# Kernel tuning notes

Hardware: AMD Instinct MI355X
Metric: run time of the kernel (lower is better)

## Reference

```python
import jax, jax.numpy as jnp
import numpy as np

N = 50000        # nodes
E_RAND = 800000  # random edges (self-loops appended -> E = 850000)
H = 8            # num_heads
D = 32           # h_feat_dim
IN = 128         # in_feat_dim
SM = 256         # sm_dim
SP = 128         # sp_dim
NEG_SLOPE = 0.2  # DGL GATv2Conv default


def setup_inputs() -> dict:
    key = jax.random.key(0)
    ks = jax.random.split(key, 16)
    s = 0.05
    self_loops = jnp.arange(N, dtype=jnp.int32)
    return {
        "sm_feats": jax.random.normal(ks[0], (N, SM), jnp.float32),
        "sp_feats": jax.random.normal(ks[1], (N, SP), jnp.float32),
        "src": jnp.concatenate([jax.random.randint(ks[2], (E_RAND,), 0, N, jnp.int32), self_loops]),
        "dst": jnp.concatenate([jax.random.randint(ks[3], (E_RAND,), 0, N, jnp.int32), self_loops]),
        # T1 / T2 linears
        "T1_w": jax.random.normal(ks[4], (SM, IN), jnp.float32) * s,
        "T1_b": jnp.zeros((IN,), jnp.float32),
        "T2_w": jax.random.normal(ks[5], (SP, IN), jnp.float32) * s,
        "T2_b": jnp.zeros((IN,), jnp.float32),
        # GATv2 layer 1: in = 2*IN
        "g1_src_w": jax.random.normal(ks[6], (2 * IN, H * D), jnp.float32) * s,
        "g1_dst_w": jax.random.normal(ks[7], (2 * IN, H * D), jnp.float32) * s,
        "g1_attn": jax.random.normal(ks[8], (H, D), jnp.float32) * s,
        "g1_bias": jnp.zeros((H * D,), jnp.float32),
        # GATv2 layer 2: in = D (after head-mean)
        "g2_src_w": jax.random.normal(ks[9], (D, H * D), jnp.float32) * s,
        "g2_dst_w": jax.random.normal(ks[10], (D, H * D), jnp.float32) * s,
        "g2_attn": jax.random.normal(ks[11], (H, D), jnp.float32) * s,
        "g2_bias": jnp.zeros((H * D,), jnp.float32),
    }


def gatv2_conv(x, src, dst, w_src, w_dst, attn, bias):
    # DGL GATv2Conv (share_weights=False, bias=True, no residual/activation)
    feat_src = (x @ w_src).reshape(-1, H, D)   # [N,H,D]
    feat_dst = (x @ w_dst).reshape(-1, H, D)   # [N,H,D]
    e = jax.nn.leaky_relu(feat_src[src] + feat_dst[dst], NEG_SLOPE)  # [E,H,D]
    score = jnp.einsum('ehd,hd->eh', e, attn)  # [E,H]
    # edge softmax over incoming edges per destination (self-loops ensure non-empty)
    smax = jax.ops.segment_max(score, dst, num_segments=N)           # [N,H]
    ex = jnp.exp(score - smax[dst])
    denom = jax.ops.segment_sum(ex, dst, num_segments=N)             # [N,H]
    alpha = ex / denom[dst]                                          # [E,H]
    out = jax.ops.segment_sum(alpha[:, :, None] * feat_src[src], dst, num_segments=N)  # [N,H,D]
    return out + bias.reshape(1, H, D)


def reference(sm_feats, sp_feats, src, dst,
              T1_w, T1_b, T2_w, T2_b,
              g1_src_w, g1_dst_w, g1_attn, g1_bias,
              g2_src_w, g2_dst_w, g2_attn, g2_bias):
    in_feat = jnp.concatenate([sm_feats @ T1_w + T1_b,
                               sp_feats @ T2_w + T2_b], axis=1)      # [N, 2*IN]
    h = gatv2_conv(in_feat, src, dst, g1_src_w, g1_dst_w, g1_attn, g1_bias)
    h = jax.nn.elu(h).mean(axis=1)                                   # [N, D]
    h = gatv2_conv(h, src, dst, g2_src_w, g2_dst_w, g2_attn, g2_bias)
    return h.mean(axis=1)                                            # [N, D]
```

## Files before the change

### kernel.cpp

```cpp
#include <hip/hip_runtime.h>
#include <hip/hip_fp16.h>


typedef unsigned int uint32;
typedef unsigned short u16;
typedef short short8 __attribute__((ext_vector_type(8)));
typedef float f32x4 __attribute__((ext_vector_type(4)));
typedef _Float16 f16x2 __attribute__((ext_vector_type(2)));

union H2 { f16x2 v; uint32 u; };

__device__ __forceinline__ uint32 bf_rne(uint32 u) { return (u + 0x7fffu + ((u >> 16) & 1u)) >> 16; }

__device__ __forceinline__ void split_trunc(float a, float b, uint32& h, uint32& l) {
  uint32 ua = __float_as_uint(a), ub = __float_as_uint(b);
  h = __builtin_amdgcn_perm(ub, ua, 0x07060302u);
  float ra = a - __uint_as_float(ua & 0xffff0000u);
  float rb = b - __uint_as_float(ub & 0xffff0000u);
  l = __builtin_amdgcn_perm(__float_as_uint(rb), __float_as_uint(ra), 0x07060302u);
}

__device__ __forceinline__ int wave_incl_scan(int x) {
  int lane = threadIdx.x & 63;
#pragma unroll
  for (int off = 1; off < 64; off <<= 1) {
    int t = __shfl_up(x, off, 64);
    if (lane >= off) x += t;
  }
  return x;
}

__global__ __launch_bounds__(256) void k_deg(const int* __restrict__ dst, int* __restrict__ deg, int E) {
  int e = blockIdx.x * 256 + threadIdx.x;
  if (e < E) atomicAdd(&deg[dst[e]], 1);
}

__global__ __launch_bounds__(256) void k_blkscan(const int* __restrict__ in, int* __restrict__ out,
                                                 int* __restrict__ blksum, int n) {
  __shared__ int wsum[4];
  int tid = threadIdx.x;
  int i0 = blockIdx.x * 1024 + tid * 4;
  int v0 = 0, v1 = 0, v2 = 0, v3 = 0;
  if (i0 + 3 < n) {
    int4 t = *(const int4*)(in + i0);
    v0 = t.x; v1 = t.y; v2 = t.z; v3 = t.w;
  } else {
    if (i0 < n) v0 = in[i0];
    if (i0 + 1 < n) v1 = in[i0 + 1];
    if (i0 + 2 < n) v2 = in[i0 + 2];
    if (i0 + 3 < n) v3 = in[i0 + 3];
  }
  int ts = v0 + v1 + v2 + v3;
  int incl = wave_incl_scan(ts);
  int lane = tid & 63, wid = tid >> 6;
  if (lane == 63) wsum[wid] = incl;
  __syncthreads();
  if (tid == 0) {
    int a = wsum[0], b = wsum[1], c = wsum[2], d = wsum[3];
    wsum[0] = 0; wsum[1] = a; wsum[2] = a + b; wsum[3] = a + b + c;
    blksum[blockIdx.x] = a + b + c + d;
  }
  __syncthreads();
  int excl = wsum[wid] + incl - ts;
  if (i0 + 3 < n) {
    int4 o; o.x = excl; o.y = excl + v0; o.z = excl + v0 + v1; o.w = excl + v0 + v1 + v2;
    *(int4*)(out + i0) = o;
  } else {
    if (i0 < n) out[i0] = excl;
    if (i0 + 1 < n) out[i0 + 1] = excl + v0;
    if (i0 + 2 < n) out[i0 + 2] = excl + v0 + v1;
    if (i0 + 3 < n) out[i0 + 3] = excl + v0 + v1 + v2;
  }
}

__global__ void k_scan_top(int* __restrict__ bs, int G) {
  int lane = threadIdx.x;
  int base = 0;
  for (int s = 0; s < G; s += 64) {
    int i = s + lane;
    int v = (i < G) ? bs[i] : 0;
    int incl = wave_incl_scan(v);
    if (i < G) bs[i] = base + incl - v;
    base += __shfl(incl, 63, 64);
  }
}

__global__ __launch_bounds__(256) void k_addoff(int* __restrict__ rp, const int* __restrict__ bs, int n, int Etot) {
  int i = blockIdx.x * 256 + threadIdx.x;
  if (i < n) rp[i] += bs[i >> 10];
  if (i == 0) rp[n] = Etot;
}

__global__ __launch_bounds__(256) void k_fill(const int* __restrict__ src, const int* __restrict__ dst,
                                              const int* __restrict__ rp, int* __restrict__ cnt,
                                              int* __restrict__ csr_src, int E) {
  int e = blockIdx.x * 256 + threadIdx.x;
  if (e < E) {
    int d = dst[e];
    int p = rp[d] + atomicAdd(&cnt[d], 1);
    csr_src[p] = src[e];
  }
}

__global__ __launch_bounds__(256) void k_precomb(const float* __restrict__ T1w, const float* __restrict__ T1b,
                                                 const float* __restrict__ T2w, const float* __restrict__ T2b,
                                                 const float* __restrict__ G, u16* __restrict__ Bh,
                                                 u16* __restrict__ Bl, float* __restrict__ cvec, int off) {
  int r = blockIdx.x;
  int j = threadIdx.x;
  float acc = 0.f;
  if (r < 256) {
    for (int m = 0; m < 128; m++) acc += T1w[r * 128 + m] * G[m * 256 + j];
  } else if (r < 384) {
    int rr = r - 256;
    for (int m = 0; m < 128; m++) acc += T2w[rr * 128 + m] * G[(128 + m) * 256 + j];
  } else {
    for (int m = 0; m < 128; m++) acc += T1b[m] * G[m * 256 + j] + T2b[m] * G[(128 + m) * 256 + j];
    cvec[off + j] = acc;
    return;
  }
  uint32 u = __float_as_uint(acc);
  uint32 hi = bf_rne(u);
  float rest = acc - __uint_as_float(hi << 16);
  uint32 lo = __float_as_uint(rest) >> 16;
  int k = r, colabs = off + j;
  int kt = k >> 5, lq = (k >> 3) & 3, j8 = k & 7;
  int cb = colabs >> 7, colr = colabs & 127, ni = colr >> 4, lr = colr & 15;
  size_t idx = ((size_t)(((cb * 12 + kt) * 8 + ni) * 4 + lq) * 16 + lr) * 8 + j8;
  Bh[idx] = (u16)hi;
  Bl[idx] = (u16)lo;
}

__global__ __launch_bounds__(256, 4) void k_gemm(const float* __restrict__ sm, const float* __restrict__ sp,
                                                 const u16* __restrict__ Bth, const u16* __restrict__ Btl,
                                                 const float* __restrict__ cvec, __half* __restrict__ fs,
                                                 __half* __restrict__ fd, int N) {
  __shared__ u16 BH[8192];
  __shared__ u16 BL[8192];
  int tid = threadIdx.x, w = tid >> 6, l = tid & 63;
  int lr = l & 15, lq = l >> 4;
  int cb = blockIdx.x, col0 = cb * 128, row0 = blockIdx.y * 128;
  int r0 = row0 + w * 32 + lr;
  int r1 = r0 + 16;
  int c0 = r0 < N ? r0 : N - 1;
  int c1 = r1 < N ? r1 : N - 1;

  f32x4 acc[2][8];
#pragma unroll
  for (int mt = 0; mt < 2; mt++)
#pragma unroll
    for (int ni = 0; ni < 8; ni++) acc[mt][ni] = (f32x4){0.f, 0.f, 0.f, 0.f};

  for (int st = 0; st < 6; st++) {
    int koff = st * 64;
    size_t g0 = (size_t)(cb * 12 + st * 2) * 4096;
    if (st) __syncthreads();
#pragma unroll
    for (int i = 0; i < 4; i++) {
      int c = i * 256 + tid;
      *(uint4*)&BH[c * 8] = *(const uint4*)(Bth + g0 + c * 8);
      *(uint4*)&BL[c * 8] = *(const uint4*)(Btl + g0 + c * 8);
    }
    __syncthreads();
#pragma unroll
    for (int t = 0; t < 2; t++) {
      int kk = koff + t * 32;
      int ks = kk + lq * 8;
      const float* ga0 = (kk < 256) ? (sm + (size_t)c0 * 256 + ks) : (sp + (size_t)c0 * 128 + (ks - 256));
      const float* ga1 = (kk < 256) ? (sm + (size_t)c1 * 256 + ks) : (sp + (size_t)c1 * 128 + (ks - 256));
      float4 v00 = *(const float4*)(ga0);
      float4 v01 = *(const float4*)(ga0 + 4);
      float4 v10 = *(const float4*)(ga1);
      float4 v11 = *(const float4*)(ga1 + 4);
      uint4 H0, L0, H1, L1;
      split_trunc(v00.x, v00.y, H0.x, L0.x);
      split_trunc(v00.z, v00.w, H0.y, L0.y);
      split_trunc(v01.x, v01.y, H0.z, L0.z);
      split_trunc(v01.z, v01.w, H0.w, L0.w);
      split_trunc(v10.x, v10.y, H1.x, L1.x);
      split_trunc(v10.z, v10.w, H1.y, L1.y);
      split_trunc(v11.x, v11.y, H1.z, L1.z);
      split_trunc(v11.z, v11.w, H1.w, L1.w);
      short8 a0h = *(short8*)&H0, a0l = *(short8*)&L0;
      short8 a1h = *(short8*)&H1, a1l = *(short8*)&L1;
#pragma unroll
      for (int ni = 0; ni < 8; ni++) {
        int lo = ((t * 8 + ni) * 64 + l) * 8;
        short8 bh = *(const short8*)&BH[lo];
        short8 bl = *(const short8*)&BL[lo];
        acc[0][ni] = __builtin_amdgcn_mfma_f32_16x16x32_bf16(a0h, bh, acc[0][ni], 0, 0, 0);
        acc[0][ni] = __builtin_amdgcn_mfma_f32_16x16x32_bf16(a0l, bh, acc[0][ni], 0, 0, 0);
        acc[0][ni] = __builtin_amdgcn_mfma_f32_16x16x32_bf16(a0h, bl, acc[0][ni], 0, 0, 0);
        acc[1][ni] = __builtin_amdgcn_mfma_f32_16x16x32_bf16(a1h, bh, acc[1][ni], 0, 0, 0);
        acc[1][ni] = __builtin_amdgcn_mfma_f32_16x16x32_bf16(a1l, bh, acc[1][ni], 0, 0, 0);
        acc[1][ni] = __builtin_amdgcn_mfma_f32_16x16x32_bf16(a1h, bl, acc[1][ni], 0, 0, 0);
      }
    }
  }
#pragma unroll
  for (int mt = 0; mt < 2; mt++) {
    int rb = row0 + w * 32 + mt * 16 + lq * 4;
#pragma unroll
    for (int ni = 0; ni < 8; ni++) {
      int c = col0 + ni * 16 + lr;
      float cv = cvec[c];
      __half* op = fs; int cc = c;
      if (c >= 256) { op = fd; cc = c - 256; }
#pragma unroll
      for (int r = 0; r < 4; r++) {
        int rr = rb + r;
        if (rr < N) op[(size_t)rr * 256 + cc] = __float2half(acc[mt][ni][r] + cv);
      }
    }
  }
}

__global__ __launch_bounds__(256) void k_feat2(const float* __restrict__ h, const float* __restrict__ Ws,
                                               const float* __restrict__ Wd, __half* __restrict__ fs,
                                               __half* __restrict__ fd, int N) {
  int j = threadIdx.x;
  int n0 = blockIdx.x * 32;
  float ws[32], wd[32];
#pragma unroll
  for (int k = 0; k < 32; k++) {
    ws[k] = Ws[k * 256 + j];
    wd[k] = Wd[k * 256 + j];
  }
  int nend = n0 + 32; if (nend > N) nend = N;
#pragma unroll 2
  for (int n = n0; n < nend; n++) {
    const float* hr = h + (size_t)n * 32;
    float as = 0.f, ad = 0.f;
#pragma unroll
    for (int k = 0; k < 32; k++) {
      float hv = hr[k];
      as += hv * ws[k];
      ad += hv * wd[k];
    }
    fs[(size_t)n * 256 + j] = __float2half(as);
    fd[(size_t)n * 256 + j] = __float2half(ad);
  }
}

template <int FINAL>
__global__ __launch_bounds__(256) void k_edge(const uint2* __restrict__ fs, const uint2* __restrict__ fd,
                                              const int* __restrict__ csr_src, const int* __restrict__ rp,
                                              const float* __restrict__ attn, const float* __restrict__ bias,
                                              float* __restrict__ out, int N) {
  int n = blockIdx.x * 4 + (threadIdx.x >> 6);
  if (n >= N) return;
  int lane = threadIdx.x & 63;
  float4 av = ((const float4*)attn)[lane];
  H2 AV01, AV23, Y01, Y23;
  AV01.v = (f16x2){(_Float16)av.x, (_Float16)av.y};
  AV23.v = (f16x2){(_Float16)av.z, (_Float16)av.w};
  const f16x2 c02 = {(_Float16)0.2f, (_Float16)0.2f};
  uint2 yu = fd[(size_t)n * 64 + lane];
  Y01.u = yu.x; Y23.u = yu.y;
  int beg = rp[n], end = rp[n + 1];
  float den0 = 0.f, den1 = 0.f;
  float4 acc0 = {0.f, 0.f, 0.f, 0.f}, acc1 = {0.f, 0.f, 0.f, 0.f};
  int e = beg;
  for (; e + 2 <= end; e += 2) {
    int s0 = csr_src[e], s1 = csr_src[e + 1];
    uint2 xu0 = fs[(size_t)s0 * 64 + lane];
    uint2 xu1 = fs[(size_t)s1 * 64 + lane];
    H2 Xa, Xb, Xc, Xd;
    Xa.u = xu0.x; Xb.u = xu0.y; Xc.u = xu1.x; Xd.u = xu1.y;
    f16x2 ea0 = Xa.v + Y01.v, eb0 = Xb.v + Y23.v;
    f16x2 ea1 = Xc.v + Y01.v, eb1 = Xd.v + Y23.v;
    f16x2 ta0 = __builtin_elementwise_max(ea0, ea0 * c02);
    f16x2 tb0 = __builtin_elementwise_max(eb0, eb0 * c02);
    f16x2 ta1 = __builtin_elementwise_max(ea1, ea1 * c02);
    f16x2 tb1 = __builtin_elementwise_max(eb1, eb1 * c02);
    float p0 = __builtin_amdgcn_fdot2(ta0, AV01.v, 0.f, false);
    float p1 = __builtin_amdgcn_fdot2(ta1, AV01.v, 0.f, false);
    p0 = __builtin_amdgcn_fdot2(tb0, AV23.v, p0, false);
    p1 = __builtin_amdgcn_fdot2(tb1, AV23.v, p1, false);
    p0 += __shfl_xor(p0, 1, 64); p1 += __shfl_xor(p1, 1, 64);
    p0 += __shfl_xor(p0, 2, 64); p1 += __shfl_xor(p1, 2, 64);
    p0 += __shfl_xor(p0, 4, 64); p1 += __shfl_xor(p1, 4, 64);
    float w0 = __expf(p0), w1 = __expf(p1);
    den0 += w0; den1 += w1;
    acc0.x += w0 * (float)Xa.v.x; acc0.y += w0 * (float)Xa.v.y;
    acc0.z += w0 * (float)Xb.v.x; acc0.w += w0 * (float)Xb.v.y;
    acc1.x += w1 * (float)Xc.v.x; acc1.y += w1 * (float)Xc.v.y;
    acc1.z += w1 * (float)Xd.v.x; acc1.w += w1 * (float)Xd.v.y;
  }
  if (e < end) {
    int s0 = csr_src[e];
    uint2 xu0 = fs[(size_t)s0 * 64 + lane];
    H2 Xa, Xb; Xa.u = xu0.x; Xb.u = xu0.y;
    f16x2 ea0 = Xa.v + Y01.v, eb0 = Xb.v + Y23.v;
    f16x2 ta0 = __builtin_elementwise_max(ea0, ea0 * c02);
    f16x2 tb0 = __builtin_elementwise_max(eb0, eb0 * c02);
    float p0 = __builtin_amdgcn_fdot2(ta0, AV01.v, 0.f, false);
    p0 = __builtin_amdgcn_fdot2(tb0, AV23.v, p0, false);
    p0 += __shfl_xor(p0, 1, 64);
    p0 += __shfl_xor(p0, 2, 64);
    p0 += __shfl_xor(p0, 4, 64);
    float w0 = __expf(p0);
    den0 += w0;
    acc0.x += w0 * (float)Xa.v.x; acc0.y += w0 * (float)Xa.v.y;
    acc0.z += w0 * (float)Xb.v.x; acc0.w += w0 * (float)Xb.v.y;
  }
  float4 acc = {acc0.x + acc1.x, acc0.y + acc1.y, acc0.z + acc1.z, acc0.w + acc1.w};
  float invd = 1.f / (den0 + den1);
  float4 b = ((const float4*)bias)[lane];
  acc.x = acc.x * invd + b.x;
  acc.y = acc.y * invd + b.y;
  acc.z = acc.z * invd + b.z;
  acc.w = acc.w * invd + b.w;
  if (!FINAL) {
    acc.x = acc.x > 0.f ? acc.x : expm1f(acc.x);
    acc.y = acc.y > 0.f ? acc.y : expm1f(acc.y);
    acc.z = acc.z > 0.f ? acc.z : expm1f(acc.z);
    acc.w = acc.w > 0.f ? acc.w : expm1f(acc.w);
  }
#pragma unroll
  for (int mask = 8; mask <= 32; mask <<= 1) {
    acc.x += __shfl_xor(acc.x, mask, 64);
    acc.y += __shfl_xor(acc.y, mask, 64);
    acc.z += __shfl_xor(acc.z, mask, 64);
    acc.w += __shfl_xor(acc.w, mask, 64);
  }
  if (lane < 8) {
    float4 o = {acc.x * 0.125f, acc.y * 0.125f, acc.z * 0.125f, acc.w * 0.125f};
    ((float4*)out)[(size_t)n * 8 + lane] = o;
  }
}

extern "C" void kernel_launch(void* const* d_in, const int* in_sizes, int n_in,
                              void* d_out, int out_size, void* d_ws, size_t ws_size,
                              hipStream_t stream) {
  const float* sm  = (const float*)d_in[0];
  const float* sp  = (const float*)d_in[1];
  const int*   src = (const int*)d_in[2];
  const int*   dst = (const int*)d_in[3];
  const float* T1w = (const float*)d_in[4];
  const float* T1b = (const float*)d_in[5];
  const float* T2w = (const float*)d_in[6];
  const float* T2b = (const float*)d_in[7];
  const float* g1sw = (const float*)d_in[8];
  const float* g1dw = (const float*)d_in[9];
  const float* g1a  = (const float*)d_in[10];
  const float* g1b  = (const float*)d_in[11];
  const float* g2sw = (const float*)d_in[12];
  const float* g2dw = (const float*)d_in[13];
  const float* g2a  = (const float*)d_in[14];
  const float* g2b  = (const float*)d_in[15];
  const int N = in_sizes[1] / 128;
  const int E = in_sizes[2];
  float* out = (float*)d_out;

  size_t off = 0;
  char* wsb = (char*)d_ws;
  auto alloc = [&](size_t bytes) -> void* {
    void* p = wsb + off;
    off += (bytes + 255) & ~(size_t)255;
    return p;
  };
  u16* Bth = (u16*)alloc((size_t)512 * 384 * 2);
  u16* Btl = (u16*)alloc((size_t)512 * 384 * 2);
  float* cvec  = (float*)alloc(512 * 4);
  int* deg     = (int*)alloc((size_t)N * 4);
  int* cnt     = (int*)alloc((size_t)N * 4);
  int* row_ptr = (int*)alloc((size_t)(N + 1) * 4);
  int* blksum  = (int*)alloc(4096 * 4);
  int* csr_src = (int*)alloc((size_t)E * 4);
  __half* fs   = (__half*)alloc((size_t)N * 256 * 2);
  __half* fd   = (__half*)alloc((size_t)N * 256 * 2);
  float* hmid  = (float*)alloc((size_t)N * 32 * 4);
  (void)ws_size; (void)n_in; (void)out_size;

  (void)hipMemsetAsync(deg, 0, (size_t)N * 4, stream);
  (void)hipMemsetAsync(cnt, 0, (size_t)N * 4, stream);

  k_deg<<<(E + 255) / 256, 256, 0, stream>>>(dst, deg, E);
  int nblk = (N + 1023) / 1024;
  k_blkscan<<<nblk, 256, 0, stream>>>(deg, row_ptr, blksum, N);
  k_scan_top<<<1, 64, 0, stream>>>(blksum, nblk);
  k_addoff<<<(N + 255) / 256, 256, 0, stream>>>(row_ptr, blksum, N, E);
  k_fill<<<(E + 255) / 256, 256, 0, stream>>>(src, dst, row_ptr, cnt, csr_src, E);

  k_precomb<<<385, 256, 0, stream>>>(T1w, T1b, T2w, T2b, g1sw, Bth, Btl, cvec, 0);
  k_precomb<<<385, 256, 0, stream>>>(T1w, T1b, T2w, T2b, g1dw, Bth, Btl, cvec, 256);

  dim3 ggrid(4, (N + 127) / 128);
  k_gemm<<<ggrid, 256, 0, stream>>>(sm, sp, Bth, Btl, cvec, fs, fd, N);
  k_edge<0><<<(N + 3) / 4, 256, 0, stream>>>((const uint2*)fs, (const uint2*)fd, csr_src, row_ptr, g1a, g1b, hmid, N);

  k_feat2<<<(N + 31) / 32, 256, 0, stream>>>(hmid, g2sw, g2dw, fs, fd, N);
  k_edge<1><<<(N + 3) / 4, 256, 0, stream>>>((const uint2*)fs, (const uint2*)fd, csr_src, row_ptr, g2a, g2b, out, N);
}
```

Baseline: 508.7 us.

## Double-buffer GEMM with async LDS loads, swizzle blocks, prefetch edge gathers

The GEMM now double-buffers the B tiles in shared memory and fills them with global_load_lds, while register-prefetching the next A stage so loads overlap the MFMA work. Its launch becomes a 1D grid with a swizzled block-to-tile mapping that groups the four column blocks of nearby row blocks, and occupancy is lowered to 2 blocks per CU. The edge kernel gathers four source rows ahead of the compute for the previous four, hiding gather latency at the cost of more registers. The two precombine launches are merged into one.

New measurement: 498.5 us. -2.0%, faster.

```diff
diff --git a/kernel.cpp b/kernel.cpp
--- a/kernel.cpp
+++ b/kernel.cpp
@@ -104,9 +104,13 @@
 
 __global__ __launch_bounds__(256) void k_precomb(const float* __restrict__ T1w, const float* __restrict__ T1b,
                                                  const float* __restrict__ T2w, const float* __restrict__ T2b,
-                                                 const float* __restrict__ G, u16* __restrict__ Bh,
-                                                 u16* __restrict__ Bl, float* __restrict__ cvec, int off) {
-  int r = blockIdx.x;
+                                                 const float* __restrict__ G1, const float* __restrict__ G2,
+                                                 u16* __restrict__ Bh, u16* __restrict__ Bl,
+                                                 float* __restrict__ cvec) {
+  int bb = blockIdx.x;
+  const float* G = (bb < 385) ? G1 : G2;
+  int off = (bb < 385) ? 0 : 256;
+  int r = (bb < 385) ? bb : bb - 385;
   int j = threadIdx.x;
   float acc = 0.f;
   if (r < 256) {
@@ -131,19 +135,33 @@
   Bl[idx] = (u16)lo;
 }
 
-__global__ __launch_bounds__(256, 4) void k_gemm(const float* __restrict__ sm, const float* __restrict__ sp,
+#define GLL(GP, LP)                                                     \
+  __builtin_amdgcn_global_load_lds(                                     \
+      (const __attribute__((address_space(1))) void*)(GP),              \
+      (__attribute__((address_space(3))) void*)(LP), 16, 0, 0)
+
+__global__ __launch_bounds__(256, 2) void k_gemm(const float* __restrict__ sm, const float* __restrict__ sp,
                                                  const u16* __restrict__ Bth, const u16* __restrict__ Btl,
                                                  const float* __restrict__ cvec, __half* __restrict__ fs,
                                                  __half* __restrict__ fd, int N) {
-  __shared__ u16 BH[8192];
-  __shared__ u16 BL[8192];
+  __shared__ u16 BH[2][8192];
+  __shared__ u16 BL[2][8192];
   int tid = threadIdx.x, w = tid >> 6, l = tid & 63;
   int lr = l & 15, lq = l >> 4;
-  int cb = blockIdx.x, col0 = cb * 128, row0 = blockIdx.y * 128;
+  int L = blockIdx.x;
+  int x = L & 7, m = L >> 3;
+  int cb = m & 3;
+  int rb = x + 8 * (m >> 2);
+  int col0 = cb * 128, row0 = rb * 128;
+  if (row0 >= N) return;
   int r0 = row0 + w * 32 + lr;
   int r1 = r0 + 16;
   int c0 = r0 < N ? r0 : N - 1;
   int c1 = r1 < N ? r1 : N - 1;
+  const float* psm0 = sm + (size_t)c0 * 256 + lq * 8;
+  const float* psm1 = sm + (size_t)c1 * 256 + lq * 8;
+  const float* psp0 = sp + (size_t)c0 * 128 + lq * 8;
+  const float* psp1 = sp + (size_t)c1 * 128 + lq * 8;
 
   f32x4 acc[2][8];
 #pragma unroll
@@ -151,55 +169,74 @@
 #pragma unroll
     for (int ni = 0; ni < 8; ni++) acc[mt][ni] = (f32x4){0.f, 0.f, 0.f, 0.f};
 
+#define STAGE_B(S, BUF)                                                 \
+  {                                                                     \
+    size_t g0 = (size_t)(cb * 12 + (S)*2) * 4096;                       \
+    _Pragma("unroll") for (int i = 0; i < 4; i++) {                     \
+      int c = i * 256 + tid;                                            \
+      int lb = (i * 4 + w) * 512;                                       \
+      GLL(Bth + g0 + (size_t)c * 8, &BH[BUF][lb]);                      \
+      GLL(Btl + g0 + (size_t)c * 8, &BL[BUF][lb]);                      \
+    }                                                                   \
+  }
+
+#define LOADA(P, D)                                                     \
+  {                                                                     \
+    const float* _g0 = ((P) < 8) ? (psm0 + (P)*32) : (psp0 + ((P)-8) * 32); \
+    const float* _g1 = ((P) < 8) ? (psm1 + (P)*32) : (psp1 + ((P)-8) * 32); \
+    D[0] = *(const float4*)_g0;                                         \
+    D[1] = *(const float4*)(_g0 + 4);                                   \
+    D[2] = *(const float4*)_g1;                                         \
+    D[3] = *(const float4*)(_g1 + 4);                                   \
+  }
+
+#define COMP(T, BUF, D)                                                 \
+  {                                                                     \
+    uint4 H0, L0, H1, L1;                                               \
+    split_trunc(D[0].x, D[0].y, H0.x, L0.x);                            \
+    split_trunc(D[0].z, D[0].w, H0.y, L0.y);                            \
+    split_trunc(D[1].x, D[1].y, H0.z, L0.z);                            \
+    split_trunc(D[1].z, D[1].w, H0.w, L0.w);                            \
+    split_trunc(D[2].x, D[2].y, H1.x, L1.x);                            \
+    split_trunc(D[2].z, D[2].w, H1.y, L1.y);                            \
+    split_trunc(D[3].x, D[3].y, H1.z, L1.z);                            \
+    split_trunc(D[3].z, D[3].w, H1.w, L1.w);                            \
+    short8 a0h = *(short8*)&H0, a0l = *(short8*)&L0;                    \
+    short8 a1h = *(short8*)&H1, a1l = *(short8*)&L1;                    \
+    _Pragma("unroll") for (int ni = 0; ni < 8; ni++) {                  \
+      int lo = (((T)*8 + ni) * 64 + l) * 8;                             \
+      short8 bh = *(const short8*)&BH[BUF][lo];                         \
+      short8 bl = *(const short8*)&BL[BUF][lo];                         \
+      acc[0][ni] = __builtin_amdgcn_mfma_f32_16x16x32_bf16(a0h, bh, acc[0][ni], 0, 0, 0); \
+      acc[0][ni] = __builtin_amdgcn_mfma_f32_16x16x32_bf16(a0l, bh, acc[0][ni], 0, 0, 0); \
+      acc[0][ni] = __builtin_amdgcn_mfma_f32_16x16x32_bf16(a0h, bl, acc[0][ni], 0, 0, 0); \
+      acc[1][ni] = __builtin_amdgcn_mfma_f32_16x16x32_bf16(a1h, bh, acc[1][ni], 0, 0, 0); \
+      acc[1][ni] = __builtin_amdgcn_mfma_f32_16x16x32_bf16(a1l, bh, acc[1][ni], 0, 0, 0); \
+      acc[1][ni] = __builtin_amdgcn_mfma_f32_16x16x32_bf16(a1h, bl, acc[1][ni], 0, 0, 0); \
+    }                                                                   \
+  }
+
+  float4 A[2][8];
+  STAGE_B(0, 0);
+  LOADA(0, A[0]);
+  LOADA(1, (A[0] + 4));
+
+#pragma unroll
   for (int st = 0; st < 6; st++) {
-    int koff = st * 64;
-    size_t g0 = (size_t)(cb * 12 + st * 2) * 4096;
-    if (st) __syncthreads();
-#pragma unroll
-    for (int i = 0; i < 4; i++) {
-      int c = i * 256 + tid;
-      *(uint4*)&BH[c * 8] = *(const uint4*)(Bth + g0 + c * 8);
-      *(uint4*)&BL[c * 8] = *(const uint4*)(Btl + g0 + c * 8);
+    const int cu = st & 1, nx = cu ^ 1;
+    __syncthreads();
+    if (st < 5) {
+      STAGE_B(st + 1, nx);
+      LOADA(2 * st + 2, A[nx]);
+      LOADA(2 * st + 3, (A[nx] + 4));
     }
-    __syncthreads();
-#pragma unroll
-    for (int t = 0; t < 2; t++) {
-      int kk = koff + t * 32;
-      int ks = kk + lq * 8;
-      const float* ga0 = (kk < 256) ? (sm + (size_t)c0 * 256 + ks) : (sp + (size_t)c0 * 128 + (ks - 256));
-      const float* ga1 = (kk < 256) ? (sm + (size_t)c1 * 256 + ks) : (sp + (size_t)c1 * 128 + (ks - 256));
-      float4 v00 = *(const float4*)(ga0);
-      float4 v01 = *(const float4*)(ga0 + 4);
-      float4 v10 = *(const float4*)(ga1);
-      float4 v11 = *(const float4*)(ga1 + 4);
-      uint4 H0, L0, H1, L1;
-      split_trunc(v00.x, v00.y, H0.x, L0.x);
-      split_trunc(v00.z, v00.w, H0.y, L0.y);
-      split_trunc(v01.x, v01.y, H0.z, L0.z);
-      split_trunc(v01.z, v01.w, H0.w, L0.w);
-      split_trunc(v10.x, v10.y, H1.x, L1.x);
-      split_trunc(v10.z, v10.w, H1.y, L1.y);
-      split_trunc(v11.x, v11.y, H1.z, L1.z);
-      split_trunc(v11.z, v11.w, H1.w, L1.w);
-      short8 a0h = *(short8*)&H0, a0l = *(short8*)&L0;
-      short8 a1h = *(short8*)&H1, a1l = *(short8*)&L1;
-#pragma unroll
-      for (int ni = 0; ni < 8; ni++) {
-        int lo = ((t * 8 + ni) * 64 + l) * 8;
-        short8 bh = *(const short8*)&BH[lo];
-        short8 bl = *(const short8*)&BL[lo];
-        acc[0][ni] = __builtin_amdgcn_mfma_f32_16x16x32_bf16(a0h, bh, acc[0][ni], 0, 0, 0);
-        acc[0][ni] = __builtin_amdgcn_mfma_f32_16x16x32_bf16(a0l, bh, acc[0][ni], 0, 0, 0);
-        acc[0][ni] = __builtin_amdgcn_mfma_f32_16x16x32_bf16(a0h, bl, acc[0][ni], 0, 0, 0);
-        acc[1][ni] = __builtin_amdgcn_mfma_f32_16x16x32_bf16(a1h, bh, acc[1][ni], 0, 0, 0);
-        acc[1][ni] = __builtin_amdgcn_mfma_f32_16x16x32_bf16(a1l, bh, acc[1][ni], 0, 0, 0);
-        acc[1][ni] = __builtin_amdgcn_mfma_f32_16x16x32_bf16(a1h, bl, acc[1][ni], 0, 0, 0);
-      }
-    }
-  }
+    COMP(0, cu, A[cu]);
+    COMP(1, cu, (A[cu] + 4));
+  }
+
 #pragma unroll
   for (int mt = 0; mt < 2; mt++) {
-    int rb = row0 + w * 32 + mt * 16 + lq * 4;
+    int rbr = row0 + w * 32 + mt * 16 + lq * 4;
 #pragma unroll
     for (int ni = 0; ni < 8; ni++) {
       int c = col0 + ni * 16 + lr;
@@ -208,11 +245,14 @@
       if (c >= 256) { op = fd; cc = c - 256; }
 #pragma unroll
       for (int r = 0; r < 4; r++) {
-        int rr = rb + r;
+        int rr = rbr + r;
         if (rr < N) op[(size_t)rr * 256 + cc] = __float2half(acc[mt][ni][r] + cv);
       }
     }
   }
+#undef STAGE_B
+#undef LOADA
+#undef COMP
 }
 
 __global__ __launch_bounds__(256) void k_feat2(const float* __restrict__ h, const float* __restrict__ Ws,
@@ -260,50 +300,52 @@
   int beg = rp[n], end = rp[n + 1];
   float den0 = 0.f, den1 = 0.f;
   float4 acc0 = {0.f, 0.f, 0.f, 0.f}, acc1 = {0.f, 0.f, 0.f, 0.f};
+
+  auto edge1 = [&](uint2 xu, float& den, float4& acc) {
+    H2 Xa, Xb; Xa.u = xu.x; Xb.u = xu.y;
+    f16x2 ea = Xa.v + Y01.v, eb = Xb.v + Y23.v;
+    f16x2 ta = __builtin_elementwise_max(ea, ea * c02);
+    f16x2 tb = __builtin_elementwise_max(eb, eb * c02);
+    float p = __builtin_amdgcn_fdot2(ta, AV01.v, 0.f, false);
+    p = __builtin_amdgcn_fdot2(tb, AV23.v, p, false);
+    p += __shfl_xor(p, 1, 64);
+    p += __shfl_xor(p, 2, 64);
+    p += __shfl_xor(p, 4, 64);
+    float wgt = __expf(p);
+    den += wgt;
+    acc.x += wgt * (float)Xa.v.x; acc.y += wgt * (float)Xa.v.y;
+    acc.z += wgt * (float)Xb.v.x; acc.w += wgt * (float)Xb.v.y;
+  };
+
   int e = beg;
-  for (; e + 2 <= end; e += 2) {
-    int s0 = csr_src[e], s1 = csr_src[e + 1];
-    uint2 xu0 = fs[(size_t)s0 * 64 + lane];
-    uint2 xu1 = fs[(size_t)s1 * 64 + lane];
-    H2 Xa, Xb, Xc, Xd;
-    Xa.u = xu0.x; Xb.u = xu0.y; Xc.u = xu1.x; Xd.u = xu1.y;
-    f16x2 ea0 = Xa.v + Y01.v, eb0 = Xb.v + Y23.v;
-    f16x2 ea1 = Xc.v + Y01.v, eb1 = Xd.v + Y23.v;
-    f16x2 ta0 = __builtin_elementwise_max(ea0, ea0 * c02);
-    f16x2 tb0 = __builtin_elementwise_max(eb0, eb0 * c02);
-    f16x2 ta1 = __builtin_elementwise_max(ea1, ea1 * c02);
-    f16x2 tb1 = __builtin_elementwise_max(eb1, eb1 * c02);
-    float p0 = __builtin_amdgcn_fdot2(ta0, AV01.v, 0.f, false);
-    float p1 = __builtin_amdgcn_fdot2(ta1, AV01.v, 0.f, false);
-    p0 = __builtin_amdgcn_fdot2(tb0, AV23.v, p0, false);
-    p1 = __builtin_amdgcn_fdot2(tb1, AV23.v, p1, false);
-    p0 += __shfl_xor(p0, 1, 64); p1 += __shfl_xor(p1, 1, 64);
-    p0 += __shfl_xor(p0, 2, 64); p1 += __shfl_xor(p1, 2, 64);
-    p0 += __shfl_xor(p0, 4, 64); p1 += __shfl_xor(p1, 4, 64);
-    float w0 = __expf(p0), w1 = __expf(p1);
-    den0 += w0; den1 += w1;
-    acc0.x += w0 * (float)Xa.v.x; acc0.y += w0 * (float)Xa.v.y;
-    acc0.z += w0 * (float)Xb.v.x; acc0.w += w0 * (float)Xb.v.y;
-    acc1.x += w1 * (float)Xc.v.x; acc1.y += w1 * (float)Xc.v.y;
-    acc1.z += w1 * (float)Xd.v.x; acc1.w += w1 * (float)Xd.v.y;
-  }
-  if (e < end) {
+  int nq = (end - beg) >> 2;
+  if (nq > 0) {
+    int s0 = csr_src[e], s1 = csr_src[e + 1], s2 = csr_src[e + 2], s3 = csr_src[e + 3];
+    uint2 x0 = fs[(size_t)s0 * 64 + lane];
+    uint2 x1 = fs[(size_t)s1 * 64 + lane];
+    uint2 x2 = fs[(size_t)s2 * 64 + lane];
+    uint2 x3 = fs[(size_t)s3 * 64 + lane];
+    for (int q = 1; q < nq; q++) {
+      int b2 = e + 4 * q;
+      int t0 = csr_src[b2], t1 = csr_src[b2 + 1], t2 = csr_src[b2 + 2], t3 = csr_src[b2 + 3];
+      uint2 y0 = fs[(size_t)t0 * 64 + lane];
+      uint2 y1 = fs[(size_t)t1 * 64 + lane];
+      uint2 y2 = fs[(size_t)t2 * 64 + lane];
+      uint2 y3 = fs[(size_t)t3 * 64 + lane];
+      edge1(x0, den0, acc0); edge1(x1, den1, acc1);
+      edge1(x2, den0, acc0); edge1(x3, den1, acc1);
+      x0 = y0; x1 = y1; x2 = y2; x3 = y3;
+    }
+    edge1(x0, den0, acc0); edge1(x1, den1, acc1);
+    edge1(x2, den0, acc0); edge1(x3, den1, acc1);
+    e += 4 * nq;
+  }
+  for (; e < end; e++) {
     int s0 = csr_src[e];
-    uint2 xu0 = fs[(size_t)s0 * 64 + lane];
-    H2 Xa, Xb; Xa.u = xu0.x; Xb.u = xu0.y;
-    f16x2 ea0 = Xa.v + Y01.v, eb0 = Xb.v + Y23.v;
-    f16x2 ta0 = __builtin_elementwise_max(ea0, ea0 * c02);
-    f16x2 tb0 = __builtin_elementwise_max(eb0, eb0 * c02);
-    float p0 = __builtin_amdgcn_fdot2(ta0, AV01.v, 0.f, false);
-    p0 = __builtin_amdgcn_fdot2(tb0, AV23.v, p0, false);
-    p0 += __shfl_xor(p0, 1, 64);
-    p0 += __shfl_xor(p0, 2, 64);
-    p0 += __shfl_xor(p0, 4, 64);
-    float w0 = __expf(p0);
-    den0 += w0;
-    acc0.x += w0 * (float)Xa.v.x; acc0.y += w0 * (float)Xa.v.y;
-    acc0.z += w0 * (float)Xb.v.x; acc0.w += w0 * (float)Xb.v.y;
-  }
+    uint2 xu = fs[(size_t)s0 * 64 + lane];
+    edge1(xu, den0, acc0);
+  }
+
   float4 acc = {acc0.x + acc1.x, acc0.y + acc1.y, acc0.z + acc1.z, acc0.w + acc1.w};
   float invd = 1.f / (den0 + den1);
   float4 b = ((const float4*)bias)[lane];
@@ -383,11 +425,11 @@
   k_addoff<<<(N + 255) / 256, 256, 0, stream>>>(row_ptr, blksum, N, E);
   k_fill<<<(E + 255) / 256, 256, 0, stream>>>(src, dst, row_ptr, cnt, csr_src, E);
 
-  k_precomb<<<385, 256, 0, stream>>>(T1w, T1b, T2w, T2b, g1sw, Bth, Btl, cvec, 0);
-  k_precomb<<<385, 256, 0, stream>>>(T1w, T1b, T2w, T2b, g1dw, Bth, Btl, cvec, 256);
-
-  dim3 ggrid(4, (N + 127) / 128);
-  k_gemm<<<ggrid, 256, 0, stream>>>(sm, sp, Bth, Btl, cvec, fs, fd, N);
+  k_precomb<<<770, 256, 0, stream>>>(T1w, T1b, T2w, T2b, g1sw, g1dw, Bth, Btl, cvec);
+
+  int rbs = (N + 127) / 128;
+  int rbp = (rbs + 7) & ~7;
+  k_gemm<<<dim3(rbp * 4), 256, 0, stream>>>(sm, sp, Bth, Btl, cvec, fs, fd, N);
   k_edge<0><<<(N + 3) / 4, 256, 0, stream>>>((const uint2*)fs, (const uint2*)fd, csr_src, row_ptr, g1a, g1b, hmid, N);
 
   k_feat2<<<(N + 31) / 32, 256, 0, stream>>>(hmid, g2sw, g2dw, fs, fd, N);
```
